# Kernel optimization log

Measured on AMD Instinct MI355X. Metric: run time of the kernel, lower is better.

Reference implementation:

```python
import jax, jax.numpy as jnp
import numpy as np
from jax import lax

B, T0, H0, W0 = 8, 8, 14, 14
C, NH = 768, 8
D = C // NH            # head_dim = 96
N = T0 * H0 * W0 + 1   # 1569 tokens incl. cls
SCALE = D ** -0.5
EPS = 1e-5


def _pool_norm(xh, conv_w, ln_g, ln_b, thw, stride):
    """AttentionPool with depthwise conv3d + LayerNorm. xh: [B, NH, N, D]."""
    cls_tok, xs = xh[:, :, :1, :], xh[:, :, 1:, :]
    b, n, _, d = xs.shape
    t, h, w = thw
    # (b n) c t h w
    xs = xs.reshape(b * n, t, h, w, d).transpose(0, 4, 1, 2, 3)
    y = lax.conv_general_dilated(
        xs, conv_w, window_strides=stride,
        padding=[(1, 1), (1, 1), (1, 1)],
        feature_group_count=d,
        dimension_numbers=("NCDHW", "OIDHW", "NCDHW"))
    ot, oh, ow = y.shape[2], y.shape[3], y.shape[4]
    y = y.transpose(0, 2, 3, 4, 1).reshape(b, n, ot * oh * ow, d)
    y = jnp.concatenate([cls_tok, y], axis=2)
    mu = y.mean(-1, keepdims=True)
    var = y.var(-1, keepdims=True)
    y = (y - mu) * lax.rsqrt(var + EPS) * ln_g + ln_b
    return y, (ot, oh, ow)


def setup_inputs() -> dict:
    key = jax.random.key(0)
    ks = jax.random.split(key, 12)
    s = lambda fan: (1.0 / np.sqrt(fan))
    return {
        "x": jax.random.normal(ks[0], (B, N, C), jnp.float32),
        "W_qkv": jax.random.normal(ks[1], (C, 3 * C), jnp.float32) * s(C),
        "b_qkv": jnp.zeros((3 * C,), jnp.float32),
        "W_proj": jax.random.normal(ks[2], (C, C), jnp.float32) * s(C),
        "b_proj": jnp.zeros((C,), jnp.float32),
        "conv_q_w": jax.random.normal(ks[3], (D, 1, 3, 3, 3), jnp.float32) * s(27),
        "conv_k_w": jax.random.normal(ks[4], (D, 1, 3, 3, 3), jnp.float32) * s(27),
        "conv_v_w": jax.random.normal(ks[5], (D, 1, 3, 3, 3), jnp.float32) * s(27),
        "lnq_g": jnp.ones((D,), jnp.float32), "lnq_b": jnp.zeros((D,), jnp.float32),
        "lnk_g": jnp.ones((D,), jnp.float32), "lnk_b": jnp.zeros((D,), jnp.float32),
        "lnv_g": jnp.ones((D,), jnp.float32), "lnv_b": jnp.zeros((D,), jnp.float32),
        "t": T0, "h": H0, "w": W0,
    }


def reference(x, W_qkv, b_qkv, W_proj, b_proj,
              conv_q_w, conv_k_w, conv_v_w,
              lnq_g, lnq_b, lnk_g, lnk_b, lnv_g, lnv_b,
              t, h, w):
    thw = (int(t), int(h), int(w))
    Bx, Nx, Cx = x.shape
    qkv = x @ W_qkv + b_qkv                       # [B, N, 3C]
    qkv = qkv.reshape(Bx, Nx, 3, NH, D).transpose(2, 0, 3, 1, 4)  # qkv b h n d
    q, k, v = qkv[0], qkv[1], qkv[2]
    q, q_shape = _pool_norm(q, conv_q_w, lnq_g, lnq_b, thw, (1, 1, 1))
    k, _ = _pool_norm(k, conv_k_w, lnk_g, lnk_b, thw, (1, 2, 2))
    v, _ = _pool_norm(v, conv_v_w, lnv_g, lnv_b, thw, (1, 2, 2))
    dots = jnp.einsum("bhid,bhjd->bhij", q, k) * SCALE
    attn = jax.nn.softmax(dots, axis=-1)
    out = jnp.einsum("bhij,bhjd->bhid", attn, v)  # [B, NH, Nq, D]
    out = out.transpose(0, 2, 1, 3).reshape(Bx, -1, Cx)
    out = out @ W_proj + b_proj
    return out
```

## Files before the change

### kernel.cpp

```cpp
#include <hip/hip_runtime.h>
#include <hip/hip_bf16.h>
#include <math.h>

#define B_   8
#define NH_  8
#define D_   96
#define C_   768
#define N_   1569
#define NKV_ 393
#define M_   (B_*N_)
#define QKV1 ((size_t)B_*NH_*N_*D_)
#define QPAD 1664
#define KPAD 416
#define SCALE_ 0.10206207261596575f

using short8v = __attribute__((ext_vector_type(8))) short;
using f32x4   = __attribute__((ext_vector_type(4))) float;
using f32x2   = __attribute__((ext_vector_type(2))) float;
typedef unsigned short u16;

#define GLOAD_LDS16(g, l) __builtin_amdgcn_global_load_lds( \
    (const __attribute__((address_space(1))) void*)(g),     \
    (__attribute__((address_space(3))) void*)(l), 16, 0, 0)

static __device__ __forceinline__ u16 f2bf(float f) {
    __hip_bfloat16 b = __float2bfloat16(f);
    return *(u16*)&b;
}

static __device__ __forceinline__ unsigned xcd_swizzle(unsigned orig, unsigned nwg) {
    const unsigned qq = nwg >> 3, rr = nwg & 7;
    const unsigned xcd = orig & 7, loc = orig >> 3;
    return (xcd < rr ? xcd * (qq + 1) : rr * (qq + 1) + (xcd - rr) * qq) + loc;
}

#define PREP_CVT_B   9414
#define PREP_WQ_B    1728
#define PREP_WP_B    576
#define PREP_WT_B    31
#define PREP_ZP_B    552
#define PREP_BLOCKS  (PREP_CVT_B + PREP_WQ_B + PREP_WP_B + PREP_WT_B + PREP_ZP_B)

static __device__ __forceinline__
void tile_transpose(const float* __restrict__ W, u16* __restrict__ Wt,
                    int ncols, int n0, int k0, float* tile )
{
    const int tx = threadIdx.x & 31, ty = threadIdx.x >> 5;
    #pragma unroll
    for (int i = 0; i < 4; ++i)
        tile[(ty + i * 8) * 33 + tx] = W[(size_t)(k0 + ty + i * 8) * ncols + n0 + tx];
    __syncthreads();
    #pragma unroll
    for (int i = 0; i < 4; ++i)
        Wt[(size_t)(n0 + ty + i * 8) * 768 + k0 + tx] = f2bf(tile[tx * 33 + ty + i * 8]);
}

__global__ __launch_bounds__(256)
void prep_kernel(const float* __restrict__ x, const float* __restrict__ Wqkv,
                 const float* __restrict__ Wproj,
                 const float* __restrict__ cwq, const float* __restrict__ cwk,
                 const float* __restrict__ cwv,
                 u16* __restrict__ x16, u16* __restrict__ Wqkvt,
                 u16* __restrict__ Wprojt, float* __restrict__ cwT,
                 u16* __restrict__ vt16)
{
    __shared__ float tile[32 * 33];
    const int bid = blockIdx.x;
    const int tid = threadIdx.x;

    if (bid < PREP_CVT_B) {
        const int i = bid * 256 + tid;
        const int n4 = M_ * 768 / 4;
        if (i < n4) {
            const float4 v = ((const float4*)x)[i];
            ushort4 o;
            o.x = f2bf(v.x); o.y = f2bf(v.y); o.z = f2bf(v.z); o.w = f2bf(v.w);
            ((ushort4*)x16)[i] = o;
        }
    } else if (bid < PREP_CVT_B + PREP_WQ_B) {
        const int b2 = bid - PREP_CVT_B;
        tile_transpose(Wqkv, Wqkvt, 2304, (b2 % 72) * 32, (b2 / 72) * 32, tile);
    } else if (bid < PREP_CVT_B + PREP_WQ_B + PREP_WP_B) {
        const int b2 = bid - PREP_CVT_B - PREP_WQ_B;
        tile_transpose(Wproj, Wprojt, 768, (b2 % 24) * 32, (b2 / 24) * 32, tile);
    } else if (bid < PREP_CVT_B + PREP_WQ_B + PREP_WP_B + PREP_WT_B) {
        const int i = (bid - PREP_CVT_B - PREP_WQ_B - PREP_WP_B) * 256 + tid;
        if (i < 3 * 27 * 96) {
            const int tsr = i / 2592;
            const int r = i - tsr * 2592;
            const int tap = r / 96, ch = r - tap * 96;
            const float* src = tsr == 0 ? cwq : (tsr == 1 ? cwk : cwv);
            cwT[i] = src[ch * 27 + tap];
        }
    } else {
        const int i = (bid - PREP_CVT_B - PREP_WQ_B - PREP_WP_B - PREP_WT_B) * 256 + tid;
        const int total = 64 * 96 * (KPAD - NKV_);
        if (i < total) {
            const int j = i % (KPAD - NKV_);
            const int rest = i / (KPAD - NKV_);
            vt16[(size_t)rest * KPAD + NKV_ + j] = 0;
        }
    }
}

template<int NC, int BN, bool SCATTER>
__global__ __launch_bounds__(512, 4)
void gemm_bf16_kernel(const u16* __restrict__ A, const u16* __restrict__ Bt,
                      const float* __restrict__ bias, void* __restrict__ outp)
{
    constexpr int NXT    = NC / BN;
    constexpr int WN     = BN / 4;
    constexpr int NBF    = WN / 16;
    constexpr int BLOADS = BN / 64;

    __shared__ alignas(16) u16 As[128 * 64];
    __shared__ alignas(16) u16 Bs[BN * 64];

    const int tid  = threadIdx.x;
    const int w    = tid >> 6, lane = tid & 63;
    const int c    = lane & 15, g = lane >> 4;
    const int wm   = w >> 2, wn = w & 3;
    const int lrow = lane >> 3, lcol = lane & 7;

    const unsigned wg = xcd_swizzle(blockIdx.x, gridDim.x);
    const int m0 = (int)(wg / NXT) * 128;
    const int n0 = (int)(wg % NXT) * BN;

    f32x4 acc[4][NBF];
    #pragma unroll
    for (int i = 0; i < 4; ++i)
        #pragma unroll
        for (int j = 0; j < NBF; ++j) acc[i][j] = (f32x4){0.f, 0.f, 0.f, 0.f};

#define STAGE(K0) do {                                                           \
    _Pragma("unroll")                                                            \
    for (int it2 = 0; it2 < 2; ++it2) {                                          \
        const int rb = it2 * 64 + w * 8;                                         \
        const int row = rb + lrow;                                               \
        const int scol = (lcol ^ (row & 7)) * 8;                                 \
        int m = m0 + row; if (m >= M_) m = M_ - 1;                               \
        GLOAD_LDS16(&A[(size_t)m * 768 + (K0) + scol], &As[rb * 64]);            \
    }                                                                            \
    _Pragma("unroll")                                                            \
    for (int it2 = 0; it2 < BLOADS; ++it2) {                                     \
        const int rb = it2 * 64 + w * 8;                                         \
        const int row = rb + lrow;                                               \
        const int scol = (lcol ^ (row & 7)) * 8;                                 \
        GLOAD_LDS16(&Bt[(size_t)(n0 + row) * 768 + (K0) + scol], &Bs[rb * 64]);  \
    } } while (0)

    const int xora = (g ^ (c & 7)) * 8;
    const int xorb = ((4 + g) ^ (c & 7)) * 8;

#define KSTEP(T) do {                                                            \
    asm volatile("s_waitcnt vmcnt(0)" ::: "memory");                             \
    __builtin_amdgcn_s_barrier();                                                \
    {                                                                            \
        short8v a0[4], b0[NBF];                                                  \
        _Pragma("unroll")                                                        \
        for (int i = 0; i < 4; ++i)                                              \
            a0[i] = *(const short8v*)&As[(wm * 64 + i * 16 + c) * 64 + xora];    \
        _Pragma("unroll")                                                        \
        for (int j = 0; j < NBF; ++j)                                            \
            b0[j] = *(const short8v*)&Bs[(wn * WN + j * 16 + c) * 64 + xora];    \
        asm volatile("s_waitcnt lgkmcnt(0)" ::: "memory");                       \
        __builtin_amdgcn_sched_barrier(0);                                       \
        __builtin_amdgcn_s_setprio(1);                                           \
        _Pragma("unroll")                                                        \
        for (int i = 0; i < 4; ++i)                                              \
            _Pragma("unroll")                                                    \
            for (int j = 0; j < NBF; ++j)                                        \
                acc[i][j] = __builtin_amdgcn_mfma_f32_16x16x32_bf16(             \
                    a0[i], b0[j], acc[i][j], 0, 0, 0);                           \
        __builtin_amdgcn_s_setprio(0);                                           \
    }                                                                            \
    {                                                                            \
        short8v a1[4], b1[NBF];                                                  \
        _Pragma("unroll")                                                        \
        for (int i = 0; i < 4; ++i)                                              \
            a1[i] = *(const short8v*)&As[(wm * 64 + i * 16 + c) * 64 + xorb];    \
        _Pragma("unroll")                                                        \
        for (int j = 0; j < NBF; ++j)                                            \
            b1[j] = *(const short8v*)&Bs[(wn * WN + j * 16 + c) * 64 + xorb];    \
        asm volatile("s_waitcnt lgkmcnt(0)" ::: "memory");                       \
        __builtin_amdgcn_sched_barrier(0);                                       \
        __builtin_amdgcn_s_barrier();                                            \
        if ((T) + 1 < 12) STAGE(((T) + 1) * 64);                                 \
        __builtin_amdgcn_s_setprio(1);                                           \
        _Pragma("unroll")                                                        \
        for (int i = 0; i < 4; ++i)                                              \
            _Pragma("unroll")                                                    \
            for (int j = 0; j < NBF; ++j)                                        \
                acc[i][j] = __builtin_amdgcn_mfma_f32_16x16x32_bf16(             \
                    a1[i], b1[j], acc[i][j], 0, 0, 0);                           \
        __builtin_amdgcn_s_setprio(0);                                           \
    } } while (0)

    STAGE(0);
    #pragma unroll
    for (int t = 0; t < 12; ++t) KSTEP(t);
#undef STAGE
#undef KSTEP

    #pragma unroll
    for (int i = 0; i < 4; ++i) {
        const int mrow = m0 + wm * 64 + i * 16 + g * 4;
        #pragma unroll
        for (int j = 0; j < NBF; ++j) {
            const int ncol = n0 + wn * WN + j * 16 + c;
            const float bv = bias[ncol];
            if constexpr (SCATTER) {
                u16* out = (u16*)outp;
                const int s   = ncol / C_;
                const int rem = ncol - s * C_;
                const int hh  = rem / D_;
                const int dd  = rem - hh * D_;
                #pragma unroll
                for (int r = 0; r < 4; ++r) {
                    const int m = mrow + r;
                    if (m < M_) {
                        const int bb2 = m / N_;
                        const int n = m - bb2 * N_;
                        out[(size_t)s * QKV1 +
                            ((size_t)(bb2 * NH_ + hh) * N_ + n) * D_ + dd] = f2bf(acc[i][j][r] + bv);
                    }
                }
            } else {
                float* out = (float*)outp;
                #pragma unroll
                for (int r = 0; r < 4; ++r) {
                    const int m = mrow + r;
                    if (m < M_) out[(size_t)m * NC + ncol] = acc[i][j][r] + bv;
                }
            }
        }
    }
}

static __device__ __forceinline__ void loadx6(const u16* __restrict__ rowp,
                                              int iw, f32x2 x[3])
{
    if (iw < 0 || iw >= 14) {
        x[0] = x[1] = x[2] = (f32x2){0.f, 0.f};
        return;
    }
    const unsigned* p = (const unsigned*)(rowp + (size_t)iw * 96);
    #pragma unroll
    for (int j = 0; j < 3; ++j) {
        const unsigned u = p[j];
        x[j][0] = __uint_as_float(u << 16);
        x[j][1] = __uint_as_float(u & 0xffff0000u);
    }
}

template<int STRIDE, int OHW, int WMODE, int WO0>
static __device__ __forceinline__
void pool_task(const u16* __restrict__ in, const float* __restrict__ cwT,
               const float* __restrict__ g, const float* __restrict__ bta,
               u16* __restrict__ out, int tokstride, int bh, int to, int ho,
               float oscale)
{
    const int sl = threadIdx.x & 15;
    const u16* base = in + (size_t)bh * N_ * 96 + 6 * sl;

    f32x2 acc[7][3];
    #pragma unroll
    for (int i = 0; i < 7; ++i)
        #pragma unroll
        for (int p = 0; p < 3; ++p) acc[i][p] = (f32x2){0.f, 0.f};

    #pragma unroll
    for (int dt = 0; dt < 3; ++dt) {
        const int t = to - 1 + dt;
        if (t < 0 || t > 7) continue;
        #pragma unroll
        for (int dh = 0; dh < 3; ++dh) {
            const int h = ho * STRIDE - 1 + dh;
            if (h < 0 || h >= 14) continue;
            const int tapb = dt * 9 + dh * 3;
            f32x2 wt[3][3];
            #pragma unroll
            for (int dw = 0; dw < 3; ++dw)
                #pragma unroll
                for (int p = 0; p < 3; ++p)
                    wt[dw][p] = *(const f32x2*)&cwT[(tapb + dw) * 96 + 6 * sl + 2 * p];
            const u16* rowp = base + (size_t)(1 + t * 196 + h * 14) * 96;

            if constexpr (STRIDE == 1) {
                f32x2 xm[3], x0[3], xp[3];
                loadx6(rowp, WO0 - 1, xm);
                loadx6(rowp, WO0, x0);
                #pragma unroll
                for (int wo = 0; wo < 7; ++wo) {
                    loadx6(rowp, WO0 + wo + 1, xp);
                    #pragma unroll
                    for (int p = 0; p < 3; ++p) {
                        acc[wo][p] = __builtin_elementwise_fma(wt[0][p], xm[p], acc[wo][p]);
                        acc[wo][p] = __builtin_elementwise_fma(wt[1][p], x0[p], acc[wo][p]);
                        acc[wo][p] = __builtin_elementwise_fma(wt[2][p], xp[p], acc[wo][p]);
                        xm[p] = x0[p]; x0[p] = xp[p];
                    }
                }
            } else {
                #pragma unroll
                for (int wo = 0; wo < 7; ++wo) {
                    #pragma unroll
                    for (int dw = 0; dw < 3; ++dw) {
                        f32x2 xa[3];
                        loadx6(rowp, 2 * wo - 1 + dw, xa);
                        #pragma unroll
                        for (int p = 0; p < 3; ++p)
                            acc[wo][p] = __builtin_elementwise_fma(wt[dw][p], xa[p], acc[wo][p]);
                    }
                }
            }
        }
    }

    f32x2 gg[3], bb[3];
    #pragma unroll
    for (int p = 0; p < 3; ++p) {
        gg[p] = *(const f32x2*)&g[6 * sl + 2 * p] * oscale;
        bb[p] = *(const f32x2*)&bta[6 * sl + 2 * p] * oscale;
    }

    #pragma unroll
    for (int wo = 0; wo < 7; ++wo) {
        float s = acc[wo][0][0] + acc[wo][0][1] + acc[wo][1][0] + acc[wo][1][1]
                + acc[wo][2][0] + acc[wo][2][1];
        float sq = acc[wo][0][0] * acc[wo][0][0];
        sq = fmaf(acc[wo][0][1], acc[wo][0][1], sq);
        sq = fmaf(acc[wo][1][0], acc[wo][1][0], sq);
        sq = fmaf(acc[wo][1][1], acc[wo][1][1], sq);
        sq = fmaf(acc[wo][2][0], acc[wo][2][0], sq);
        sq = fmaf(acc[wo][2][1], acc[wo][2][1], sq);
        #pragma unroll
        for (int off = 1; off < 16; off <<= 1) {
            s  += __shfl_xor(s, off, 64);
            sq += __shfl_xor(sq, off, 64);
        }
        const float mu = s * (1.f / 96.f);
        const float rstd = rsqrtf(sq * (1.f / 96.f) - mu * mu + 1e-5f);
        const f32x2 muv = (f32x2){mu, mu};
        const int tok = 1 + (to * OHW + ho) * OHW + WO0 + wo;
        u16 yb[6];
        #pragma unroll
        for (int p = 0; p < 3; ++p) {
            const f32x2 y = (acc[wo][p] - muv) * rstd * gg[p] + bb[p];
            yb[2 * p] = f2bf(y[0]); yb[2 * p + 1] = f2bf(y[1]);
        }
        if constexpr (WMODE == 2) {
            #pragma unroll
            for (int j = 0; j < 6; ++j)
                out[((size_t)bh * 96 + 6 * sl + j) * KPAD + tok] = yb[j];
        } else {
            unsigned* op = (unsigned*)&out[((size_t)bh * tokstride + tok) * 96 + 6 * sl];
            #pragma unroll
            for (int p = 0; p < 3; ++p)
                op[p] = (unsigned)yb[2 * p] | ((unsigned)yb[2 * p + 1] << 16);
        }
    }
}

template<int WMODE>
static __device__ __forceinline__
void pool_cls_v5(const u16* __restrict__ in, const float* __restrict__ g,
                 const float* __restrict__ bta, u16* __restrict__ out,
                 int tokstride, int bh, float oscale)
{
    const int sl = threadIdx.x & 15;
    const unsigned* p = (const unsigned*)(in + (size_t)bh * N_ * 96 + 6 * sl);
    f32x2 v[3];
    #pragma unroll
    for (int j = 0; j < 3; ++j) {
        const unsigned u = p[j];
        v[j][0] = __uint_as_float(u << 16);
        v[j][1] = __uint_as_float(u & 0xffff0000u);
    }
    float s = v[0][0] + v[0][1] + v[1][0] + v[1][1] + v[2][0] + v[2][1];
    float sq = v[0][0]*v[0][0] + v[0][1]*v[0][1] + v[1][0]*v[1][0]
             + v[1][1]*v[1][1] + v[2][0]*v[2][0] + v[2][1]*v[2][1];
    #pragma unroll
    for (int off = 1; off < 16; off <<= 1) {
        s  += __shfl_xor(s, off, 64);
        sq += __shfl_xor(sq, off, 64);
    }
    const float mu = s * (1.f / 96.f);
    const float rstd = rsqrtf(sq * (1.f / 96.f) - mu * mu + 1e-5f);
    u16 yb[6];
    #pragma unroll
    for (int p2 = 0; p2 < 3; ++p2) {
        const f32x2 gg = *(const f32x2*)&g[6 * sl + 2 * p2] * oscale;
        const f32x2 bb = *(const f32x2*)&bta[6 * sl + 2 * p2] * oscale;
        const f32x2 y = (v[p2] - (f32x2){mu, mu}) * rstd * gg + bb;
        yb[2 * p2] = f2bf(y[0]); yb[2 * p2 + 1] = f2bf(y[1]);
    }
    if constexpr (WMODE == 2) {
        #pragma unroll
        for (int j = 0; j < 6; ++j)
            out[((size_t)bh * 96 + 6 * sl + j) * KPAD] = yb[j];
    } else {
        unsigned* op = (unsigned*)&out[(size_t)bh * tokstride * 96 + 6 * sl];
        #pragma unroll
        for (int p2 = 0; p2 < 3; ++p2)
            op[p2] = (unsigned)yb[2 * p2] | ((unsigned)yb[2 * p2 + 1] << 16);
    }
}

#define NTASKS 21696
__global__ __launch_bounds__(256)
void pool_ln_v5_kernel(const u16* __restrict__ qin, const u16* __restrict__ kin,
                       const u16* __restrict__ vin, const float* __restrict__ cwT,
                       const float* __restrict__ gq, const float* __restrict__ bq,
                       const float* __restrict__ gk, const float* __restrict__ bk,
                       const float* __restrict__ gv, const float* __restrict__ bv,
                       u16* __restrict__ qout, u16* __restrict__ kout,
                       u16* __restrict__ vtout)
{
    const unsigned wg = xcd_swizzle(blockIdx.x, gridDim.x);
    const int gid = (int)(wg * 16 + (threadIdx.x >> 4));
    if (gid >= NTASKS) return;

    if (gid < 14336) {
        const int chunk = gid / 7168;
        const int r = gid - chunk * 7168;
        const int ho = r % 14;
        const int to = (r / 14) & 7;
        const int bh = r / 112;
        if (chunk == 0)
            pool_task<1, 14, 0, 0>(qin, cwT, gq, bq, qout, QPAD, bh, to, ho, SCALE_);
        else
            pool_task<1, 14, 0, 7>(qin, cwT, gq, bq, qout, QPAD, bh, to, ho, SCALE_);
    } else if (gid < 17920) {
        const int r = gid - 14336;
        const int ho = r % 7;
        const int to = (r / 7) & 7;
        const int bh = r / 56;
        pool_task<2, 7, 0, 0>(kin, cwT + 2592, gk, bk, kout, KPAD, bh, to, ho, 1.f);
    } else if (gid < 21504) {
        const int r = gid - 17920;
        const int ho = r % 7;
        const int to = (r / 7) & 7;
        const int bh = r / 56;
        pool_task<2, 7, 2, 0>(vin, cwT + 5184, gv, bv, vtout, KPAD, bh, to, ho, 1.f);
    } else {
        const int r = gid - 21504;
        const int tsr = r >> 6, bh = r & 63;
        if (tsr == 0)      pool_cls_v5<0>(qin, gq, bq, qout, QPAD, bh, SCALE_);
        else if (tsr == 1) pool_cls_v5<0>(kin, gk, bk, kout, KPAD, bh, 1.f);
        else               pool_cls_v5<2>(vin, gv, bv, vtout, KPAD, bh, 1.f);
    }
}

__global__ __launch_bounds__(256)
void attn_mfma_kernel(const u16* __restrict__ Q, const u16* __restrict__ K,
                      const u16* __restrict__ VT, u16* __restrict__ Out)
{
    __shared__ alignas(16) u16 plds[4][2][512];
    const int tid  = threadIdx.x;
    const int w    = tid >> 6, lane = tid & 63;
    const int c    = lane & 15, g = lane >> 4;

    const unsigned wg = xcd_swizzle(blockIdx.x, gridDim.x);
    const int bh = (int)(wg / 13);
    const int b  = bh >> 3, hh = bh & 7;
    const int q0 = (int)(wg % 13) * 128 + w * 32;

    const size_t qbase = (size_t)bh * QPAD * 96;
    const size_t kbase = (size_t)bh * KPAD * 96;

    short8v qa[2][3];
    #pragma unroll
    for (int s2 = 0; s2 < 2; ++s2)
        #pragma unroll
        for (int kf = 0; kf < 3; ++kf)
            qa[s2][kf] = *(const short8v*)
                &Q[qbase + (size_t)(q0 + s2 * 16 + c) * 96 + kf * 32 + g * 8];

    f32x4 oacc[2][6];
    #pragma unroll
    for (int s2 = 0; s2 < 2; ++s2)
        #pragma unroll
        for (int t = 0; t < 6; ++t) oacc[s2][t] = (f32x4){0.f, 0.f, 0.f, 0.f};
    float lsum[2][4] = {{0.f,0.f,0.f,0.f},{0.f,0.f,0.f,0.f}};

    short8v kb[2][6];
#define LOADK(IDX, PR) do {                                                     \
    _Pragma("unroll")                                                           \
    for (int h = 0; h < 2; ++h)                                                 \
        _Pragma("unroll")                                                       \
        for (int kf = 0; kf < 3; ++kf)                                          \
            kb[IDX][h * 3 + kf] = *(const short8v*)                             \
                &K[kbase + (size_t)((PR) * 32 + h * 16 + c) * 96 + kf * 32 + g * 8]; \
    } while (0)

    LOADK(0, 0);

    #pragma unroll
    for (int pr = 0; pr < 13; ++pr) {
        const int cur = pr & 1, nxt = cur ^ 1;

        short8v vt[6];
        #pragma unroll
        for (int t = 0; t < 6; ++t)
            vt[t] = *(const short8v*)
                &VT[kbase + (size_t)(t * 16 + c) * KPAD + pr * 32 + g * 8];

        f32x4 sacc[2][2];
        __builtin_amdgcn_s_setprio(1);
        #pragma unroll
        for (int s2 = 0; s2 < 2; ++s2)
            #pragma unroll
            for (int h = 0; h < 2; ++h) {
                f32x4 sa = (f32x4){0.f, 0.f, 0.f, 0.f};
                sa = __builtin_amdgcn_mfma_f32_16x16x32_bf16(qa[s2][0], kb[cur][h*3+0], sa, 0, 0, 0);
                sa = __builtin_amdgcn_mfma_f32_16x16x32_bf16(qa[s2][1], kb[cur][h*3+1], sa, 0, 0, 0);
                sa = __builtin_amdgcn_mfma_f32_16x16x32_bf16(qa[s2][2], kb[cur][h*3+2], sa, 0, 0, 0);
                sacc[s2][h] = sa;
            }
        __builtin_amdgcn_s_setprio(0);

        if (pr < 12) LOADK(nxt, pr + 1);

        #pragma unroll
        for (int h = 0; h < 2; ++h) {
            const int jcol = pr * 32 + h * 16 + c;
            #pragma unroll
            for (int r = 0; r < 4; ++r) {
                float s = sacc[0][h][r];
                if (jcol >= NKV_) s = -1e30f;
                const float p = __expf(s);
                lsum[0][r] += p;
                const int q    = g * 4 + r;
                const int j    = h * 16 + c;
                const int dstL = q | ((j >> 3) << 4);
                plds[w][0][dstL * 8 + (j & 7)] = f2bf(p);
            }
        }
        asm volatile("s_waitcnt lgkmcnt(0)" ::: "memory");
        __builtin_amdgcn_sched_barrier(0);
        {
            const short8v pa0 = *(const short8v*)&plds[w][0][lane * 8];
            __builtin_amdgcn_s_setprio(1);
            #pragma unroll
            for (int t = 0; t < 6; ++t)
                oacc[0][t] = __builtin_amdgcn_mfma_f32_16x16x32_bf16(pa0, vt[t], oacc[0][t], 0, 0, 0);
            __builtin_amdgcn_s_setprio(0);
        }

        #pragma unroll
        for (int h = 0; h < 2; ++h) {
            const int jcol = pr * 32 + h * 16 + c;
            #pragma unroll
            for (int r = 0; r < 4; ++r) {
                float s = sacc[1][h][r];
                if (jcol >= NKV_) s = -1e30f;
                const float p = __expf(s);
                lsum[1][r] += p;
                const int q    = g * 4 + r;
                const int j    = h * 16 + c;
                const int dstL = q | ((j >> 3) << 4);
                plds[w][1][dstL * 8 + (j & 7)] = f2bf(p);
            }
        }
        asm volatile("s_waitcnt lgkmcnt(0)" ::: "memory");
        __builtin_amdgcn_sched_barrier(0);
        {
            const short8v pa1 = *(const short8v*)&plds[w][1][lane * 8];
            __builtin_amdgcn_s_setprio(1);
            #pragma unroll
            for (int t = 0; t < 6; ++t)
                oacc[1][t] = __builtin_amdgcn_mfma_f32_16x16x32_bf16(pa1, vt[t], oacc[1][t], 0, 0, 0);
            __builtin_amdgcn_s_setprio(0);
        }
    }
#undef LOADK

    float linv[2][4];
    #pragma unroll
    for (int s2 = 0; s2 < 2; ++s2)
        #pragma unroll
        for (int r = 0; r < 4; ++r) {
            float s = lsum[s2][r];
            s += __shfl_xor(s, 1, 64);
            s += __shfl_xor(s, 2, 64);
            s += __shfl_xor(s, 4, 64);
            s += __shfl_xor(s, 8, 64);
            linv[s2][r] = 1.f / s;
        }

    #pragma unroll
    for (int s2 = 0; s2 < 2; ++s2)
        #pragma unroll
        for (int t = 0; t < 6; ++t)
            #pragma unroll
            for (int r = 0; r < 4; ++r) {
                const int row = q0 + s2 * 16 + g * 4 + r;
                if (row < N_)
                    Out[((size_t)(b * N_ + row)) * 768 + hh * 96 + t * 16 + c] =
                        f2bf(oacc[s2][t][r] * linv[s2][r]);
            }
}

extern "C" void kernel_launch(void* const* d_in, const int* in_sizes, int n_in,
                              void* d_out, int out_size, void* d_ws, size_t ws_size,
                              hipStream_t stream)
{
    const float* x     = (const float*)d_in[0];
    const float* Wqkv  = (const float*)d_in[1];
    const float* bqkv  = (const float*)d_in[2];
    const float* Wproj = (const float*)d_in[3];
    const float* bproj = (const float*)d_in[4];
    const float* cwq   = (const float*)d_in[5];
    const float* cwk   = (const float*)d_in[6];
    const float* cwv   = (const float*)d_in[7];
    const float* lnqg  = (const float*)d_in[8];
    const float* lnqb  = (const float*)d_in[9];
    const float* lnkg  = (const float*)d_in[10];
    const float* lnkb  = (const float*)d_in[11];
    const float* lnvg  = (const float*)d_in[12];
    const float* lnvb  = (const float*)d_in[13];

    u16* ws = (u16*)d_ws;
    u16* qkv_raw = ws;
    u16* q16 = qkv_raw + 3 * QKV1;
    u16* k16 = q16 + (size_t)64 * QPAD * 96;
    u16* vt16 = k16 + (size_t)64 * KPAD * 96;
    u16* x16    = vt16 + (size_t)64 * KPAD * 96;
    u16* Wqkvt  = x16 + (size_t)M_ * 768;
    u16* Wprojt = Wqkvt + (size_t)2304 * 768;
    float* cwT  = (float*)(Wprojt + (size_t)768 * 768);
    u16* attn16 = qkv_raw;
    float* out = (float*)d_out;

    prep_kernel<<<PREP_BLOCKS, 256, 0, stream>>>(
        x, Wqkv, Wproj, cwq, cwk, cwv, x16, Wqkvt, Wprojt, cwT, vt16);

    gemm_bf16_kernel<2304, 256, true><<<99 * 9, 512, 0, stream>>>(x16, Wqkvt, bqkv, qkv_raw);

    pool_ln_v5_kernel<<<(NTASKS + 15) / 16, 256, 0, stream>>>(
        qkv_raw, qkv_raw + QKV1, qkv_raw + 2 * QKV1, cwT,
        lnqg, lnqb, lnkg, lnkb, lnvg, lnvb, q16, k16, vt16);

    attn_mfma_kernel<<<13 * 64, 256, 0, stream>>>(q16, k16, vt16, attn16);

    gemm_bf16_kernel<768, 128, false><<<99 * 6, 512, 0, stream>>>(attn16, Wprojt, bproj, out);
}
```

Before: 187.5 us.

## Double-buffer LDS tiles in bf16 GEMM with partial vmcnt waits

Converts both GEMM kernels from single-buffered static LDS to a two-stage dynamic LDS ring. Loads for step T+2 are issued while step T is computed, and the wait becomes a partial vmcnt so the newest stage's loads can stay in flight. The aim is to hide global-to-LDS latency behind MFMA work. In exchange, LDS per block doubles (up to 96 KB), which can lower occupancy below the launch-bounds target. The hardcoded vmcnt counts also have to match the exact number of issued loads.

```diff
diff --git a/kernel.cpp b/kernel.cpp
--- a/kernel.cpp
+++ b/kernel.cpp
@@ -112,9 +112,9 @@
     constexpr int WN     = BN / 4;
     constexpr int NBF    = WN / 16;
     constexpr int BLOADS = BN / 64;
-
-    __shared__ alignas(16) u16 As[128 * 64];
-    __shared__ alignas(16) u16 Bs[BN * 64];
+    constexpr int TILE_U = (128 + BN) * 64;
+
+    extern __shared__ u16 smem[];
 
     const int tid  = threadIdx.x;
     const int w    = tid >> 6, lane = tid & 63;
@@ -132,37 +132,49 @@
         #pragma unroll
         for (int j = 0; j < NBF; ++j) acc[i][j] = (f32x4){0.f, 0.f, 0.f, 0.f};
 
-#define STAGE(K0) do {                                                           \
+#define STAGE(K0, BUF) do {                                                      \
     _Pragma("unroll")                                                            \
     for (int it2 = 0; it2 < 2; ++it2) {                                          \
         const int rb = it2 * 64 + w * 8;                                         \
         const int row = rb + lrow;                                               \
         const int scol = (lcol ^ (row & 7)) * 8;                                 \
         int m = m0 + row; if (m >= M_) m = M_ - 1;                               \
-        GLOAD_LDS16(&A[(size_t)m * 768 + (K0) + scol], &As[rb * 64]);            \
+        GLOAD_LDS16(&A[(size_t)m * 768 + (K0) + scol],                           \
+                    &smem[(BUF) * TILE_U + rb * 64]);                            \
     }                                                                            \
     _Pragma("unroll")                                                            \
     for (int it2 = 0; it2 < BLOADS; ++it2) {                                     \
         const int rb = it2 * 64 + w * 8;                                         \
         const int row = rb + lrow;                                               \
         const int scol = (lcol ^ (row & 7)) * 8;                                 \
-        GLOAD_LDS16(&Bt[(size_t)(n0 + row) * 768 + (K0) + scol], &Bs[rb * 64]);  \
+        GLOAD_LDS16(&Bt[(size_t)(n0 + row) * 768 + (K0) + scol],                 \
+                    &smem[(BUF) * TILE_U + 128 * 64 + rb * 64]);                 \
     } } while (0)
 
     const int xora = (g ^ (c & 7)) * 8;
     const int xorb = ((4 + g) ^ (c & 7)) * 8;
 
 #define KSTEP(T) do {                                                            \
-    asm volatile("s_waitcnt vmcnt(0)" ::: "memory");                             \
+     \
+    if ((T) < 11) {                                                              \
+        if constexpr (BLOADS == 4)                                               \
+            asm volatile("s_waitcnt vmcnt(6)" ::: "memory");                     \
+        else                                                                     \
+            asm volatile("s_waitcnt vmcnt(4)" ::: "memory");                     \
+    } else {                                                                     \
+        asm volatile("s_waitcnt vmcnt(0)" ::: "memory");                         \
+    }                                                                            \
     __builtin_amdgcn_s_barrier();                                                \
     {                                                                            \
         short8v a0[4], b0[NBF];                                                  \
         _Pragma("unroll")                                                        \
         for (int i = 0; i < 4; ++i)                                              \
-            a0[i] = *(const short8v*)&As[(wm * 64 + i * 16 + c) * 64 + xora];    \
+            a0[i] = *(const short8v*)&smem[((T) & 1) * TILE_U +                  \
+                     (wm * 64 + i * 16 + c) * 64 + xora];                        \
         _Pragma("unroll")                                                        \
         for (int j = 0; j < NBF; ++j)                                            \
-            b0[j] = *(const short8v*)&Bs[(wn * WN + j * 16 + c) * 64 + xora];    \
+            b0[j] = *(const short8v*)&smem[((T) & 1) * TILE_U + 128 * 64 +       \
+                     (wn * WN + j * 16 + c) * 64 + xora];                        \
         asm volatile("s_waitcnt lgkmcnt(0)" ::: "memory");                       \
         __builtin_amdgcn_sched_barrier(0);                                       \
         __builtin_amdgcn_s_setprio(1);                                           \
@@ -178,14 +190,16 @@
         short8v a1[4], b1[NBF];                                                  \
         _Pragma("unroll")                                                        \
         for (int i = 0; i < 4; ++i)                                              \
-            a1[i] = *(const short8v*)&As[(wm * 64 + i * 16 + c) * 64 + xorb];    \
+            a1[i] = *(const short8v*)&smem[((T) & 1) * TILE_U +                  \
+                     (wm * 64 + i * 16 + c) * 64 + xorb];                        \
         _Pragma("unroll")                                                        \
         for (int j = 0; j < NBF; ++j)                                            \
-            b1[j] = *(const short8v*)&Bs[(wn * WN + j * 16 + c) * 64 + xorb];    \
+            b1[j] = *(const short8v*)&smem[((T) & 1) * TILE_U + 128 * 64 +       \
+                     (wn * WN + j * 16 + c) * 64 + xorb];                        \
         asm volatile("s_waitcnt lgkmcnt(0)" ::: "memory");                       \
         __builtin_amdgcn_sched_barrier(0);                                       \
         __builtin_amdgcn_s_barrier();                                            \
-        if ((T) + 1 < 12) STAGE(((T) + 1) * 64);                                 \
+        if ((T) + 2 < 12) STAGE(((T) + 2) * 64, (T) & 1);                        \
         __builtin_amdgcn_s_setprio(1);                                           \
         _Pragma("unroll")                                                        \
         for (int i = 0; i < 4; ++i)                                              \
@@ -196,7 +210,8 @@
         __builtin_amdgcn_s_setprio(0);                                           \
     } } while (0)
 
-    STAGE(0);
+    STAGE(0, 0);
+    STAGE(64, 1);
     #pragma unroll
     for (int t = 0; t < 12; ++t) KSTEP(t);
 #undef STAGE
@@ -636,7 +651,8 @@
     prep_kernel<<<PREP_BLOCKS, 256, 0, stream>>>(
         x, Wqkv, Wproj, cwq, cwk, cwv, x16, Wqkvt, Wprojt, cwT, vt16);
 
-    gemm_bf16_kernel<2304, 256, true><<<99 * 9, 512, 0, stream>>>(x16, Wqkvt, bqkv, qkv_raw);
+    gemm_bf16_kernel<2304, 256, true><<<99 * 9, 512, 98304, stream>>>(
+        x16, Wqkvt, bqkv, qkv_raw);
 
     pool_ln_v5_kernel<<<(NTASKS + 15) / 16, 256, 0, stream>>>(
         qkv_raw, qkv_raw + QKV1, qkv_raw + 2 * QKV1, cwT,
@@ -644,5 +660,6 @@
 
     attn_mfma_kernel<<<13 * 64, 256, 0, stream>>>(q16, k16, vt16, attn16);
 
-    gemm_bf16_kernel<768, 128, false><<<99 * 6, 512, 0, stream>>>(attn16, Wprojt, bproj, out);
-}
+    gemm_bf16_kernel<768, 128, false><<<99 * 6, 512, 65536, stream>>>(
+        attn16, Wprojt, bproj, out);
+}
```

Result: slower. 218.5 us (+16.5%).
